# Performance work log

Measured on AMD Instinct MI355X. Metric: run time of the kernel, lower is better.

Reference implementation:

```python
import jax, jax.numpy as jnp
import numpy as np

H = 128  # hidden_dim


def setup_inputs() -> dict:
    key = jax.random.key(0)
    k1, k2, k3 = jax.random.split(key, 3)
    N = 1024
    return {
        "node_emb": jax.random.normal(k1, (N, H), dtype=jnp.float32),
        "W1": jax.random.normal(k2, (2 * H, H), dtype=jnp.float32) * 0.05,
        "b1": jnp.zeros((H,), dtype=jnp.float32),
        "W2": jax.random.normal(k3, (H, 1), dtype=jnp.float32) * 0.05,
        "b2": jnp.zeros((1,), dtype=jnp.float32),
    }


def reference(node_emb, W1, b1, W2, b2):
    # L2 normalize rows (torch F.normalize: x / max(||x||, eps))
    norm = jnp.sqrt(jnp.sum(node_emb * node_emb, axis=-1, keepdims=True))
    e = node_emb / jnp.maximum(norm, 1e-12)  # (N, H)
    # adj[i, j] = mlp(cat(e_i, e_j)); split W1 so we never materialize (N,N,2H)
    left = e @ W1[:H]    # (N, H) contribution of e_i
    right = e @ W1[H:]   # (N, H) contribution of e_j
    h = jax.nn.relu(left[:, None, :] + right[None, :, :] + b1)  # (N, N, H)
    logits = jnp.einsum("ijh,h->ij", h, W2[:, 0]) + b2[0]       # (N, N)
    return jax.nn.softmax(logits, axis=-1)
```

## Files before the change

kernel.cpp:

```cpp
#include <hip/hip_runtime.h>

#define H 128
#define N 1024

__global__ __launch_bounds__(512) void prep_kernel(
    const float* __restrict__ x, const float* __restrict__ W1,
    const float* __restrict__ b1, const float* __restrict__ W2,
    float* __restrict__ Lp, float* __restrict__ Rt, float* __restrict__ c)
{
    constexpr int PF = 8;
    __shared__ float e_s[4][H];
    __shared__ float cred[4][2];
    const int t = threadIdx.x;
    const int i0 = blockIdx.x * 4;

    if (t < 256) {
        const int row = t >> 6, lane = t & 63;
        const float2 v = *reinterpret_cast<const float2*>(&x[(i0 + row) * H + 2 * lane]);
        float s = v.x * v.x + v.y * v.y;
#pragma unroll
        for (int off = 32; off; off >>= 1) s += __shfl_xor(s, off);
        const float rn = 1.0f / fmaxf(sqrtf(s), 1e-12f);
        e_s[row][2 * lane]     = v.x * rn;
        e_s[row][2 * lane + 1] = v.y * rn;
    }
    __syncthreads();

    const int h = t & (H - 1);
    const int q = t >> 7;
    const int r0 = (q & 1) * 2;
    const float* Wb = W1 + (q >= 2 ? H * H : 0) + h;

    float acc0 = 0.f, acc1 = 0.f;
    float wbuf[PF];
#pragma unroll
    for (int p = 0; p < PF; ++p) wbuf[p] = Wb[p * H];

    for (int kb = 0; kb < H - PF; kb += PF) {
#pragma unroll
        for (int p = 0; p < PF; ++p) {
            const float w = wbuf[p];
            wbuf[p] = Wb[(kb + p + PF) * H];
            acc0 = fmaf(e_s[r0][kb + p],     w, acc0);
            acc1 = fmaf(e_s[r0 + 1][kb + p], w, acc1);
        }
    }
#pragma unroll
    for (int p = 0; p < PF; ++p) {
        const int k = H - PF + p;
        acc0 = fmaf(e_s[r0][k],     wbuf[p], acc0);
        acc1 = fmaf(e_s[r0 + 1][k], wbuf[p], acc1);
    }

    const float w2h = W2[h];
    if (q < 2) {
        const float bb = b1[h];
        Lp[(i0 + r0) * H + h]     = w2h * (acc0 + bb);
        Lp[(i0 + r0 + 1) * H + h] = w2h * (acc1 + bb);
    } else {
        const float v0 = w2h * acc0, v1 = w2h * acc1;
        Rt[h * N + (i0 + r0)]     = v0;
        Rt[h * N + (i0 + r0 + 1)] = v1;
        float s0 = v0, s1 = v1;
#pragma unroll
        for (int off = 32; off; off >>= 1) {
            s0 += __shfl_xor(s0, off);
            s1 += __shfl_xor(s1, off);
        }
        const int wv = t >> 6;
        if ((t & 63) == 0) { cred[wv - 4][0] = s0; cred[wv - 4][1] = s1; }
    }
    __syncthreads();
    if (t < 4) {
        const int r = t;
        c[i0 + r] = 0.5f * (cred[(r >> 1) * 2][r & 1] + cred[(r >> 1) * 2 + 1][r & 1]);
    }
}

__global__ __launch_bounds__(512) void adj_kernel(
    const float* __restrict__ Lp, const float* __restrict__ Rt,
    const float* __restrict__ W2, const float* __restrict__ c,
    float* __restrict__ out)
{
    constexpr int II = 4, PF = 16;
    __shared__ float LsT[H][4];
    __shared__ float sgn[H];
    __shared__ float red_m[II][8];
    __shared__ float red_s[II][8];

    const int t = threadIdx.x;
    const int lane = t & 63, wave = t >> 6;
    const int i0 = blockIdx.x * II;
    const int j0 = t * 2;

    if (t < H) {
        sgn[t] = (W2[t] >= 0.f) ? 0.5f : -0.5f;
        float4 lv;
        lv.x = Lp[(i0 + 0) * H + t];
        lv.y = Lp[(i0 + 1) * H + t];
        lv.z = Lp[(i0 + 2) * H + t];
        lv.w = Lp[(i0 + 3) * H + t];
        *reinterpret_cast<float4*>(&LsT[t][0]) = lv;
    }
    const float2 cj = *reinterpret_cast<const float2*>(&c[j0]);
    __syncthreads();

    float accx[II], accy[II];
#pragma unroll
    for (int ii = 0; ii < II; ++ii) { accx[ii] = cj.x; accy[ii] = cj.y; }

    float2 rbuf[PF];
#pragma unroll
    for (int p = 0; p < PF; ++p)
        rbuf[p] = *reinterpret_cast<const float2*>(&Rt[p * N + j0]);

    for (int hb = 0; hb < H - PF; hb += PF) {
#pragma unroll
        for (int p = 0; p < PF; ++p) {
            const int h = hb + p;
            const float2 r = rbuf[p];
            rbuf[p] = *reinterpret_cast<const float2*>(&Rt[(h + PF) * N + j0]);
            const float4 lv = *reinterpret_cast<const float4*>(&LsT[h][0]);
            const float s = sgn[h];
            const float* lp = &lv.x;
#pragma unroll
            for (int ii = 0; ii < II; ++ii) {
                accx[ii] = fmaf(s, fabsf(lp[ii] + r.x), accx[ii]);
                accy[ii] = fmaf(s, fabsf(lp[ii] + r.y), accy[ii]);
            }
        }
    }
#pragma unroll
    for (int p = 0; p < PF; ++p) {
        const int h = H - PF + p;
        const float2 r = rbuf[p];
        const float4 lv = *reinterpret_cast<const float4*>(&LsT[h][0]);
        const float s = sgn[h];
        const float* lp = &lv.x;
#pragma unroll
        for (int ii = 0; ii < II; ++ii) {
            accx[ii] = fmaf(s, fabsf(lp[ii] + r.x), accx[ii]);
            accy[ii] = fmaf(s, fabsf(lp[ii] + r.y), accy[ii]);
        }
    }

#pragma unroll
    for (int ii = 0; ii < II; ++ii) {
        float m = fmaxf(accx[ii], accy[ii]);
#pragma unroll
        for (int off = 32; off; off >>= 1) m = fmaxf(m, __shfl_xor(m, off));
        if (lane == 0) red_m[ii][wave] = m;
    }
    __syncthreads();

    float mm[II];
#pragma unroll
    for (int ii = 0; ii < II; ++ii) {
        float m = red_m[ii][0];
#pragma unroll
        for (int w = 1; w < 8; ++w) m = fmaxf(m, red_m[ii][w]);
        mm[ii] = m;
    }

#pragma unroll
    for (int ii = 0; ii < II; ++ii) {
        accx[ii] = expf(accx[ii] - mm[ii]);
        accy[ii] = expf(accy[ii] - mm[ii]);
        float s = accx[ii] + accy[ii];
#pragma unroll
        for (int off = 32; off; off >>= 1) s += __shfl_xor(s, off);
        if (lane == 0) red_s[ii][wave] = s;
    }
    __syncthreads();

#pragma unroll
    for (int ii = 0; ii < II; ++ii) {
        float s = red_s[ii][0];
#pragma unroll
        for (int w = 1; w < 8; ++w) s += red_s[ii][w];
        const float r = 1.0f / s;
        float2 o;
        o.x = accx[ii] * r;
        o.y = accy[ii] * r;
        *reinterpret_cast<float2*>(&out[(i0 + ii) * N + j0]) = o;
    }
}

extern "C" void kernel_launch(void* const* d_in, const int* in_sizes, int n_in,
                              void* d_out, int out_size, void* d_ws, size_t ws_size,
                              hipStream_t stream) {
    const float* x  = (const float*)d_in[0];
    const float* W1 = (const float*)d_in[1];
    const float* b1 = (const float*)d_in[2];
    const float* W2 = (const float*)d_in[3];
    float* out = (float*)d_out;

    float* Lp = (float*)d_ws;
    float* Rt = Lp + N * H;
    float* cc = Rt + H * N;

    prep_kernel<<<N / 4, 512, 0, stream>>>(x, W1, b1, W2, Lp, Rt, cc);
    adj_kernel<<<N / 4, 512, 0, stream>>>(Lp, Rt, W2, cc, out);
}
```

Measured before the change: 27.91 us.

## Split hidden dim across waves with register-resident L rows and LDS partial reduction

The adj kernel now has each wave own a 32-wide slice of the hidden dimension and a 512-column half of j. The four L rows and sign factors for that slice stay in registers, and each thread handles 8 columns using float4 loads of Rt. Partial sums go to a 64KB shared buffer and are reduced across the four h-slice waves before the softmax. This removes per-iteration LDS reads of L and widens global loads, at the cost of larger shared memory use, an extra reduction pass and barrier, and higher register pressure under launch_bounds(512,2).

```diff
diff --git a/kernel.cpp b/kernel.cpp
--- a/kernel.cpp
+++ b/kernel.cpp
@@ -77,75 +77,110 @@
     }
 }
 
-__global__ __launch_bounds__(512) void adj_kernel(
+__global__ __launch_bounds__(512, 2) void adj_kernel(
     const float* __restrict__ Lp, const float* __restrict__ Rt,
     const float* __restrict__ W2, const float* __restrict__ c,
     float* __restrict__ out)
 {
-    constexpr int II = 4, PF = 16;
-    __shared__ float LsT[H][4];
-    __shared__ float sgn[H];
-    __shared__ float red_m[II][8];
-    __shared__ float red_s[II][8];
+    __shared__ float part[8][4][512];
+    __shared__ float red_m[4][8];
+    __shared__ float red_s[4][8];
 
     const int t = threadIdx.x;
     const int lane = t & 63, wave = t >> 6;
-    const int i0 = blockIdx.x * II;
-    const int j0 = t * 2;
-
-    if (t < H) {
-        sgn[t] = (W2[t] >= 0.f) ? 0.5f : -0.5f;
-        float4 lv;
-        lv.x = Lp[(i0 + 0) * H + t];
-        lv.y = Lp[(i0 + 1) * H + t];
-        lv.z = Lp[(i0 + 2) * H + t];
-        lv.w = Lp[(i0 + 3) * H + t];
-        *reinterpret_cast<float4*>(&LsT[t][0]) = lv;
-    }
+    const int i0 = blockIdx.x * 4;
+    const int tau = wave >> 2;
+    const int omg = wave & 3;
+    const int hbase = 32 * omg;
+    const int jb = tau * 512 + 4 * lane;
+
+    float a[4][32];
+#pragma unroll
+    for (int r = 0; r < 4; ++r) {
+        const float4* ap = reinterpret_cast<const float4*>(&Lp[(i0 + r) * H + hbase]);
+#pragma unroll
+        for (int q = 0; q < 8; ++q) {
+            const float4 v = ap[q];
+            a[r][4 * q + 0] = v.x; a[r][4 * q + 1] = v.y;
+            a[r][4 * q + 2] = v.z; a[r][4 * q + 3] = v.w;
+        }
+    }
+    float sg[32];
+    {
+        const float4* wp = reinterpret_cast<const float4*>(&W2[hbase]);
+#pragma unroll
+        for (int q = 0; q < 8; ++q) {
+            const float4 wv = wp[q];
+            sg[4 * q + 0] = (wv.x >= 0.f) ? 0.5f : -0.5f;
+            sg[4 * q + 1] = (wv.y >= 0.f) ? 0.5f : -0.5f;
+            sg[4 * q + 2] = (wv.z >= 0.f) ? 0.5f : -0.5f;
+            sg[4 * q + 3] = (wv.w >= 0.f) ? 0.5f : -0.5f;
+        }
+    }
+
+    float4 acc[4][2];
+#pragma unroll
+    for (int r = 0; r < 4; ++r)
+#pragma unroll
+        for (int k = 0; k < 2; ++k) { acc[r][k].x = 0.f; acc[r][k].y = 0.f;
+                                      acc[r][k].z = 0.f; acc[r][k].w = 0.f; }
+
+    const float* Rp = Rt + hbase * N + jb;
+    float4 rb[2][2];
+    rb[0][0] = *reinterpret_cast<const float4*>(Rp);
+    rb[0][1] = *reinterpret_cast<const float4*>(Rp + 256);
+    rb[1][0] = *reinterpret_cast<const float4*>(Rp + N);
+    rb[1][1] = *reinterpret_cast<const float4*>(Rp + N + 256);
+
+#pragma unroll
+    for (int hh = 0; hh < 32; ++hh) {
+        const float4 r0 = rb[hh & 1][0];
+        const float4 r1 = rb[hh & 1][1];
+        if (hh + 2 < 32) {
+            rb[hh & 1][0] = *reinterpret_cast<const float4*>(Rp + (hh + 2) * N);
+            rb[hh & 1][1] = *reinterpret_cast<const float4*>(Rp + (hh + 2) * N + 256);
+        }
+        const float s = sg[hh];
+#pragma unroll
+        for (int r = 0; r < 4; ++r) {
+            const float av = a[r][hh];
+            acc[r][0].x = fmaf(s, fabsf(av + r0.x), acc[r][0].x);
+            acc[r][0].y = fmaf(s, fabsf(av + r0.y), acc[r][0].y);
+            acc[r][0].z = fmaf(s, fabsf(av + r0.z), acc[r][0].z);
+            acc[r][0].w = fmaf(s, fabsf(av + r0.w), acc[r][0].w);
+            acc[r][1].x = fmaf(s, fabsf(av + r1.x), acc[r][1].x);
+            acc[r][1].y = fmaf(s, fabsf(av + r1.y), acc[r][1].y);
+            acc[r][1].z = fmaf(s, fabsf(av + r1.z), acc[r][1].z);
+            acc[r][1].w = fmaf(s, fabsf(av + r1.w), acc[r][1].w);
+        }
+    }
+
+#pragma unroll
+    for (int r = 0; r < 4; ++r) {
+        *reinterpret_cast<float4*>(&part[wave][r][4 * lane])       = acc[r][0];
+        *reinterpret_cast<float4*>(&part[wave][r][4 * lane + 256]) = acc[r][1];
+    }
+    __syncthreads();
+
+    const int j0 = 2 * t;
+    const int tj = j0 >> 9;
+    const int jl = j0 & 511;
     const float2 cj = *reinterpret_cast<const float2*>(&c[j0]);
-    __syncthreads();
-
-    float accx[II], accy[II];
-#pragma unroll
-    for (int ii = 0; ii < II; ++ii) { accx[ii] = cj.x; accy[ii] = cj.y; }
-
-    float2 rbuf[PF];
-#pragma unroll
-    for (int p = 0; p < PF; ++p)
-        rbuf[p] = *reinterpret_cast<const float2*>(&Rt[p * N + j0]);
-
-    for (int hb = 0; hb < H - PF; hb += PF) {
-#pragma unroll
-        for (int p = 0; p < PF; ++p) {
-            const int h = hb + p;
-            const float2 r = rbuf[p];
-            rbuf[p] = *reinterpret_cast<const float2*>(&Rt[(h + PF) * N + j0]);
-            const float4 lv = *reinterpret_cast<const float4*>(&LsT[h][0]);
-            const float s = sgn[h];
-            const float* lp = &lv.x;
-#pragma unroll
-            for (int ii = 0; ii < II; ++ii) {
-                accx[ii] = fmaf(s, fabsf(lp[ii] + r.x), accx[ii]);
-                accy[ii] = fmaf(s, fabsf(lp[ii] + r.y), accy[ii]);
-            }
-        }
-    }
-#pragma unroll
-    for (int p = 0; p < PF; ++p) {
-        const int h = H - PF + p;
-        const float2 r = rbuf[p];
-        const float4 lv = *reinterpret_cast<const float4*>(&LsT[h][0]);
-        const float s = sgn[h];
-        const float* lp = &lv.x;
-#pragma unroll
-        for (int ii = 0; ii < II; ++ii) {
-            accx[ii] = fmaf(s, fabsf(lp[ii] + r.x), accx[ii]);
-            accy[ii] = fmaf(s, fabsf(lp[ii] + r.y), accy[ii]);
-        }
-    }
-
-#pragma unroll
-    for (int ii = 0; ii < II; ++ii) {
+    float accx[4], accy[4];
+#pragma unroll
+    for (int r = 0; r < 4; ++r) {
+        float sx = 0.f, sy = 0.f;
+#pragma unroll
+        for (int w = 0; w < 4; ++w) {
+            const float2 p = *reinterpret_cast<const float2*>(&part[4 * tj + w][r][jl]);
+            sx += p.x; sy += p.y;
+        }
+        accx[r] = sx + cj.x;
+        accy[r] = sy + cj.y;
+    }
+
+#pragma unroll
+    for (int ii = 0; ii < 4; ++ii) {
         float m = fmaxf(accx[ii], accy[ii]);
 #pragma unroll
         for (int off = 32; off; off >>= 1) m = fmaxf(m, __shfl_xor(m, off));
@@ -153,9 +188,9 @@
     }
     __syncthreads();
 
-    float mm[II];
-#pragma unroll
-    for (int ii = 0; ii < II; ++ii) {
+    float mm[4];
+#pragma unroll
+    for (int ii = 0; ii < 4; ++ii) {
         float m = red_m[ii][0];
 #pragma unroll
         for (int w = 1; w < 8; ++w) m = fmaxf(m, red_m[ii][w]);
@@ -163,7 +198,7 @@
     }
 
 #pragma unroll
-    for (int ii = 0; ii < II; ++ii) {
+    for (int ii = 0; ii < 4; ++ii) {
         accx[ii] = expf(accx[ii] - mm[ii]);
         accy[ii] = expf(accy[ii] - mm[ii]);
         float s = accx[ii] + accy[ii];
@@ -174,7 +209,7 @@
     __syncthreads();
 
 #pragma unroll
-    for (int ii = 0; ii < II; ++ii) {
+    for (int ii = 0; ii < 4; ++ii) {
         float s = red_s[ii][0];
 #pragma unroll
         for (int w = 1; w < 8; ++w) s += red_s[ii][w];
```

New measurement: 27.68 us. About the same (-0.8%).
